# Optimization experiments

Measured on AMD Instinct MI355X. Metric: run time of the kernel, lower is better.

## Reference

```python
import jax, jax.numpy as jnp
import numpy as np

BATCH = 4096
DIM = 256
TEMP = 0.5
COS_EPS = 1e-8  # torch.nn.CosineSimilarity default eps


def setup_inputs() -> dict:
    key = jax.random.key(0)
    k1, k2 = jax.random.split(key)
    zis = jax.random.normal(k1, (BATCH, DIM), dtype=jnp.float32)
    zjs = jax.random.normal(k2, (BATCH, DIM), dtype=jnp.float32)
    return {"zis": zis, "zjs": zjs}


def reference(zis, zjs):
    n = zis.shape[0]  # batch_size
    # representations = cat([zjs, zis]) -> (2N, D)
    reps = jnp.concatenate([zjs, zis], axis=0)
    # cosine similarity matrix: dot / max(|x||y|, eps)  (matches torch CosineSimilarity)
    norms = jnp.linalg.norm(reps, axis=-1)  # (2N,)
    sim = (reps @ reps.T) / jnp.maximum(norms[:, None] * norms[None, :], COS_EPS)  # (2N, 2N)
    # positives: diag at offset +N (rows 0..N-1) then offset -N (rows N..2N-1)
    pos = jnp.concatenate([jnp.diagonal(sim, n), jnp.diagonal(sim, -n)])  # (2N,)
    # CE with label 0 over [pos, negatives]: negatives = row minus {diag, positive};
    # logsumexp([pos] + negatives) == logsumexp(row with only the self-diagonal masked),
    # since the positive appears exactly once in the row.
    two_n = 2 * n
    logits = sim / TEMP
    logits = jnp.where(jnp.eye(two_n, dtype=bool), -jnp.inf, logits)
    lse = jax.nn.logsumexp(logits, axis=-1)  # (2N,)
    loss = jnp.sum(lse - pos / TEMP)  # CrossEntropyLoss(reduction='sum')
    return loss / two_n
```

## Files before the change

kernel.cpp:

```cpp
#include <hip/hip_runtime.h>
#include <hip/hip_bf16.h>

#define TWO_N  8192
#define N_HALF 4096
#define DIMS   256

typedef __bf16 bf16x8 __attribute__((ext_vector_type(8)));
typedef float  f32x4  __attribute__((ext_vector_type(4)));
typedef unsigned short ushort8v __attribute__((ext_vector_type(8)));

__device__ __forceinline__ float fast_exp2(float x) {
#if __has_builtin(__builtin_amdgcn_exp2f)
    return __builtin_amdgcn_exp2f(x);
#else
    float r; asm("v_exp_f32 %0, %1" : "=v"(r) : "v"(x)); return r;
#endif
}

#define GLOAD_LDS16(g, l)                                                      \
    __builtin_amdgcn_global_load_lds(                                          \
        (const __attribute__((address_space(1))) unsigned int*)(g),            \
        (__attribute__((address_space(3))) unsigned int*)(l), 16, 0, 0)

__global__ __launch_bounds__(256) void nrm_kernel(const float* __restrict__ zis,
                                                  const float* __restrict__ zjs,
                                                  unsigned short* __restrict__ swz)
{
    const int tid = threadIdx.x;
    const int l32 = tid & 31;
    const int row = blockIdx.x * 8 + (tid >> 5);
    const int k0  = l32 * 8;

    const float* src = (row < N_HALF) ? (zjs + (size_t)row * DIMS)
                                      : (zis + (size_t)(row - N_HALF) * DIMS);
    const float4 v0 = reinterpret_cast<const float4*>(src + k0)[0];
    const float4 v1 = reinterpret_cast<const float4*>(src + k0 + 4)[0];
    float ss = v0.x * v0.x + v0.y * v0.y + v0.z * v0.z + v0.w * v0.w
             + v1.x * v1.x + v1.y * v1.y + v1.z * v1.z + v1.w * v1.w;
#pragma unroll
    for (int m = 1; m < 32; m <<= 1) ss += __shfl_xor(ss, m, 64);
    const float inv = rsqrtf(ss) * 1.69864360045f;

    const float vals[8] = {v0.x, v0.y, v0.z, v0.w, v1.x, v1.y, v1.z, v1.w};
    ushort8v o;
#pragma unroll
    for (int j = 0; j < 8; ++j) {
        __hip_bfloat16 b = __float2bfloat16(vals[j] * inv);
        o[j] = *reinterpret_cast<unsigned short*>(&b);
    }
    const int chunk = ((row >> 4) * 8 + (l32 >> 2)) * 64 + (l32 & 3) * 16 + (row & 15);
    *reinterpret_cast<ushort8v*>(swz + (size_t)chunk * 8) = o;
}

__global__ __launch_bounds__(512, 2) void ntx_kernel(const __bf16* __restrict__ swz,
                                                     float* __restrict__ rowsum_part,
                                                     float* __restrict__ pos_part)
{
    __shared__ __bf16 abuf[2][32768];

    const int lane = threadIdx.x & 63;
    const int wave = threadIdx.x >> 6;
    const int l15  = lane & 15;
    const int quad = lane >> 4;

    const int rg     = blockIdx.x & 15;
    const int cs     = blockIdx.x >> 4;
    const int wr0    = rg * 512 + wave * 64;
    const int p0     = wr0 ^ N_HALF;

    auto stage = [&](int buf, int c) {
        const __bf16* gsrc = swz + (size_t)(cs * 32 + c * 8 + wave) * 4096 + lane * 8;
#pragma unroll
        for (int h = 0; h < 8; ++h)
            GLOAD_LDS16(gsrc + h * 512, &abuf[buf][wave * 4096 + h * 512]);
    };

    stage(0, 0);

    bf16x8 bfrag[4][8];
#pragma unroll
    for (int t = 0; t < 4; ++t) {
        const __bf16* bp = swz + (size_t)((wr0 >> 4) + t) * 4096 + lane * 8;
#pragma unroll
        for (int kk = 0; kk < 8; ++kk)
            bfrag[t][kk] = *reinterpret_cast<const bf16x8*>(bp + kk * 512);
    }

    float sum_exp[4] = {0.f, 0.f, 0.f, 0.f};
    float pos_acc = 0.f;

    asm volatile("s_waitcnt vmcnt(0)" ::: "memory");
    __syncthreads();

    int cur = 0;
    for (int c = 0; c < 4; ++c) {
        if (c < 3) stage(cur ^ 1, c + 1);

        const int cc_base = cs * 512 + c * 128;

        auto compute = [&](const bf16x8* af, int it) {
            const int c0 = cc_base + it * 16;
            f32x4 acc[4] = {{0.f, 0.f, 0.f, 0.f}, {0.f, 0.f, 0.f, 0.f},
                            {0.f, 0.f, 0.f, 0.f}, {0.f, 0.f, 0.f, 0.f}};
#pragma unroll
            for (int kk = 0; kk < 8; ++kk) {
#pragma unroll
                for (int t = 0; t < 4; ++t)
                    acc[t] = __builtin_amdgcn_mfma_f32_16x16x32_bf16(
                        af[kk], bfrag[t][kk], acc[t], 0, 0, 0);
            }
            const bool special = (c0 < wr0 + 64 && c0 + 16 > wr0) ||
                                 (c0 < p0 + 64 && c0 + 16 > p0);
            if (!special) {
#pragma unroll
                for (int t = 0; t < 4; ++t)
#pragma unroll
                    for (int j = 0; j < 4; ++j)
                        sum_exp[t] += fast_exp2(acc[t][j]);
            } else {
#pragma unroll
                for (int t = 0; t < 4; ++t) {
                    const int r = wr0 + t * 16 + l15;
#pragma unroll
                    for (int j = 0; j < 4; ++j) {
                        const int col = c0 + quad * 4 + j;
                        const float e = fast_exp2(acc[t][j]);
                        sum_exp[t] += (col == r) ? 0.f : e;
                        if (col == (r ^ N_HALF)) pos_acc += acc[t][j];
                    }
                }
            }
        };

        bf16x8 a0[8], a1[8];
#pragma unroll
        for (int kk = 0; kk < 8; ++kk)
            a0[kk] = *reinterpret_cast<const bf16x8*>(&abuf[cur][kk * 512 + lane * 8]);

        for (int it = 0; it < 8; it += 2) {
#pragma unroll
            for (int kk = 0; kk < 8; ++kk)
                a1[kk] = *reinterpret_cast<const bf16x8*>(
                    &abuf[cur][(it + 1) * 4096 + kk * 512 + lane * 8]);
            compute(a0, it);
            if (it + 2 < 8) {
#pragma unroll
                for (int kk = 0; kk < 8; ++kk)
                    a0[kk] = *reinterpret_cast<const bf16x8*>(
                        &abuf[cur][(it + 2) * 4096 + kk * 512 + lane * 8]);
            }
            compute(a1, it + 1);
        }

        asm volatile("s_waitcnt vmcnt(0)" ::: "memory");
        __syncthreads();
        cur ^= 1;
    }

#pragma unroll
    for (int t = 0; t < 4; ++t) {
        float s = sum_exp[t];
        s += __shfl_xor(s, 16, 64);
        s += __shfl_xor(s, 32, 64);
        if (lane < 16)
            rowsum_part[(size_t)cs * TWO_N + wr0 + t * 16 + lane] = s;
    }

#pragma unroll
    for (int m = 1; m < 64; m <<= 1) pos_acc += __shfl_xor(pos_acc, m, 64);
    if (lane == 0) pos_part[blockIdx.x * 8 + wave] = pos_acc;
}

__global__ __launch_bounds__(1024) void fin1_kernel(const float* __restrict__ rowsum_part,
                                                    const float* __restrict__ pos_part,
                                                    float* __restrict__ block_part)
{
    __shared__ float red[16];
    const int t = threadIdx.x;
    const int r = blockIdx.x * 1024 + t;
    float acc = 0.f;
#pragma unroll
    for (int cs = 0; cs < 16; ++cs)
        acc += rowsum_part[(size_t)cs * TWO_N + r];
    float v = logf(acc);
    if (r < 2048)
        v -= 0.69314718055994531f * pos_part[r];
#pragma unroll
    for (int m = 1; m < 64; m <<= 1) v += __shfl_xor(v, m, 64);
    if ((t & 63) == 0) red[t >> 6] = v;
    __syncthreads();
    if (t == 0) {
        float s = 0.f;
#pragma unroll
        for (int w = 0; w < 16; ++w) s += red[w];
        block_part[blockIdx.x] = s;
    }
}

__global__ void fin2_kernel(const float* __restrict__ block_part, float* __restrict__ out)
{
    if (threadIdx.x == 0) {
        float s = 0.f;
#pragma unroll
        for (int i = 0; i < 8; ++i) s += block_part[i];
        out[0] = s / (float)TWO_N;
    }
}

extern "C" void kernel_launch(void* const* d_in, const int* in_sizes, int n_in,
                              void* d_out, int out_size, void* d_ws, size_t ws_size,
                              hipStream_t stream)
{
    const float* zis = (const float*)d_in[0];
    const float* zjs = (const float*)d_in[1];

    unsigned short* swz = (unsigned short*)d_ws;
    float* rowsum_part  = (float*)((char*)d_ws + (size_t)TWO_N * DIMS * sizeof(unsigned short));
    float* pos_part     = rowsum_part + (size_t)16 * TWO_N;
    float* block_part   = pos_part + 2048;

    nrm_kernel<<<TWO_N / 8, 256, 0, stream>>>(zis, zjs, swz);
    ntx_kernel<<<256, 512, 0, stream>>>((const __bf16*)swz, rowsum_part, pos_part);
    fin1_kernel<<<8, 1024, 0, stream>>>(rowsum_part, pos_part, block_part);
    fin2_kernel<<<1, 64, 0, stream>>>(block_part, (float*)d_out);
}
```

Measured before the change: 92.09 us.

## Switch similarity GEMM to 32x32x16 MFMA with matching swizzled bf16 layout

Replaces the 16x16x32 bf16 MFMA tiles with 32x32x16 MFMA tiles. Each wave now computes two 32x32 output blocks per column group, and the staged A columns are reused across both. The normalization kernel writes a new 32-row-group swizzled layout that matches the bigger MFMA operand fragments, and the diagonal/positive masking and row-sum reductions are remapped to the 32x32 accumulator layout. The aim is fewer MFMA instructions and less LDS fragment traffic per output, at the cost of more accumulator registers (two f32x16 plus 32 per-lane partial sums), which may pressure occupancy.

```diff
diff --git a/kernel.cpp b/kernel.cpp
--- a/kernel.cpp
+++ b/kernel.cpp
@@ -6,7 +6,7 @@
 #define DIMS   256
 
 typedef __bf16 bf16x8 __attribute__((ext_vector_type(8)));
-typedef float  f32x4  __attribute__((ext_vector_type(4)));
+typedef float  f32x16 __attribute__((ext_vector_type(16)));
 typedef unsigned short ushort8v __attribute__((ext_vector_type(8)));
 
 __device__ __forceinline__ float fast_exp2(float x) {
@@ -48,8 +48,9 @@
         __hip_bfloat16 b = __float2bfloat16(vals[j] * inv);
         o[j] = *reinterpret_cast<unsigned short*>(&b);
     }
-    const int chunk = ((row >> 4) * 8 + (l32 >> 2)) * 64 + (l32 & 3) * 16 + (row & 15);
-    *reinterpret_cast<ushort8v*>(swz + (size_t)chunk * 8) = o;
+    const size_t addr = ((size_t)((row >> 5) * 16 + (l32 >> 1)) * 64
+                         + (l32 & 1) * 32 + (row & 31)) * 8;
+    *reinterpret_cast<ushort8v*>(swz + addr) = o;
 }
 
 __global__ __launch_bounds__(512, 2) void ntx_kernel(const __bf16* __restrict__ swz,
@@ -60,33 +61,35 @@
 
     const int lane = threadIdx.x & 63;
     const int wave = threadIdx.x >> 6;
-    const int l15  = lane & 15;
-    const int quad = lane >> 4;
-
-    const int rg     = blockIdx.x & 15;
-    const int cs     = blockIdx.x >> 4;
-    const int wr0    = rg * 512 + wave * 64;
-    const int p0     = wr0 ^ N_HALF;
+    const int half = lane >> 5;
+    const int cl31 = lane & 31;
+
+    const int rg   = blockIdx.x & 15;
+    const int cs   = blockIdx.x >> 4;
+    const int wr0  = rg * 512 + wave * 64;
+    const int p0   = wr0 ^ N_HALF;
+    const int g0   = wr0 >> 5;
 
     auto stage = [&](int buf, int c) {
-        const __bf16* gsrc = swz + (size_t)(cs * 32 + c * 8 + wave) * 4096 + lane * 8;
+        const __bf16* gsrc = swz + ((size_t)(cs * 256 + c * 64 + wave * 8)) * 512 + lane * 8;
 #pragma unroll
         for (int h = 0; h < 8; ++h)
-            GLOAD_LDS16(gsrc + h * 512, &abuf[buf][wave * 4096 + h * 512]);
+            GLOAD_LDS16(gsrc + h * 512, &abuf[buf][(wave * 8 + h) * 512]);
     };
 
     stage(0, 0);
 
-    bf16x8 bfrag[4][8];
-#pragma unroll
-    for (int t = 0; t < 4; ++t) {
-        const __bf16* bp = swz + (size_t)((wr0 >> 4) + t) * 4096 + lane * 8;
-#pragma unroll
-        for (int kk = 0; kk < 8; ++kk)
-            bfrag[t][kk] = *reinterpret_cast<const bf16x8*>(bp + kk * 512);
-    }
-
-    float sum_exp[4] = {0.f, 0.f, 0.f, 0.f};
+    bf16x8 bfrag[2][16];
+#pragma unroll
+    for (int t = 0; t < 2; ++t)
+#pragma unroll
+        for (int ks = 0; ks < 16; ++ks)
+            bfrag[t][ks] = *reinterpret_cast<const bf16x8*>(
+                swz + (size_t)((g0 + t) * 16 + ks) * 512 + lane * 8);
+
+    float sums0[16], sums1[16];
+#pragma unroll
+    for (int g = 0; g < 16; ++g) { sums0[g] = 0.f; sums1[g] = 0.f; }
     float pos_acc = 0.f;
 
     asm volatile("s_waitcnt vmcnt(0)" ::: "memory");
@@ -96,60 +99,58 @@
     for (int c = 0; c < 4; ++c) {
         if (c < 3) stage(cur ^ 1, c + 1);
 
-        const int cc_base = cs * 512 + c * 128;
-
-        auto compute = [&](const bf16x8* af, int it) {
-            const int c0 = cc_base + it * 16;
-            f32x4 acc[4] = {{0.f, 0.f, 0.f, 0.f}, {0.f, 0.f, 0.f, 0.f},
-                            {0.f, 0.f, 0.f, 0.f}, {0.f, 0.f, 0.f, 0.f}};
-#pragma unroll
-            for (int kk = 0; kk < 8; ++kk) {
-#pragma unroll
-                for (int t = 0; t < 4; ++t)
-                    acc[t] = __builtin_amdgcn_mfma_f32_16x16x32_bf16(
-                        af[kk], bfrag[t][kk], acc[t], 0, 0, 0);
+        for (int cg = 0; cg < 4; ++cg) {
+            const int c0 = cs * 512 + c * 128 + cg * 32;
+            const __bf16* ab = &abuf[cur][cg * 16 * 512 + lane * 8];
+
+            f32x16 acc0, acc1;
+#pragma unroll
+            for (int g = 0; g < 16; ++g) { acc0[g] = 0.f; acc1[g] = 0.f; }
+
+            bf16x8 a[8];
+#pragma unroll
+            for (int ks = 0; ks < 8; ++ks)
+                a[ks] = *reinterpret_cast<const bf16x8*>(ab + ks * 512);
+#pragma unroll
+            for (int ks = 0; ks < 8; ++ks) {
+                acc0 = __builtin_amdgcn_mfma_f32_32x32x16_bf16(a[ks], bfrag[0][ks], acc0, 0, 0, 0);
+                acc1 = __builtin_amdgcn_mfma_f32_32x32x16_bf16(a[ks], bfrag[1][ks], acc1, 0, 0, 0);
             }
-            const bool special = (c0 < wr0 + 64 && c0 + 16 > wr0) ||
-                                 (c0 < p0 + 64 && c0 + 16 > p0);
+#pragma unroll
+            for (int ks = 0; ks < 8; ++ks)
+                a[ks] = *reinterpret_cast<const bf16x8*>(ab + (8 + ks) * 512);
+#pragma unroll
+            for (int ks = 0; ks < 8; ++ks) {
+                acc0 = __builtin_amdgcn_mfma_f32_32x32x16_bf16(a[ks], bfrag[0][8 + ks], acc0, 0, 0, 0);
+                acc1 = __builtin_amdgcn_mfma_f32_32x32x16_bf16(a[ks], bfrag[1][8 + ks], acc1, 0, 0, 0);
+            }
+
+            const bool special = (c0 < wr0 + 64 && c0 + 32 > wr0) ||
+                                 (c0 < p0 + 64 && c0 + 32 > p0);
             if (!special) {
 #pragma unroll
-                for (int t = 0; t < 4; ++t)
-#pragma unroll
-                    for (int j = 0; j < 4; ++j)
-                        sum_exp[t] += fast_exp2(acc[t][j]);
+                for (int g = 0; g < 16; ++g) {
+                    sums0[g] += fast_exp2(acc0[g]);
+                    sums1[g] += fast_exp2(acc1[g]);
+                }
             } else {
-#pragma unroll
-                for (int t = 0; t < 4; ++t) {
-                    const int r = wr0 + t * 16 + l15;
-#pragma unroll
-                    for (int j = 0; j < 4; ++j) {
-                        const int col = c0 + quad * 4 + j;
-                        const float e = fast_exp2(acc[t][j]);
-                        sum_exp[t] += (col == r) ? 0.f : e;
-                        if (col == (r ^ N_HALF)) pos_acc += acc[t][j];
+                const int r0 = wr0 + cl31;
+                const int r1 = wr0 + 32 + cl31;
+#pragma unroll
+                for (int g = 0; g < 16; ++g) {
+                    const int col = c0 + (g & 3) + 8 * (g >> 2) + 4 * half;
+                    {
+                        const float e = fast_exp2(acc0[g]);
+                        sums0[g] += (col == r0) ? 0.f : e;
+                        if (col == (r0 ^ N_HALF)) pos_acc += acc0[g];
+                    }
+                    {
+                        const float e = fast_exp2(acc1[g]);
+                        sums1[g] += (col == r1) ? 0.f : e;
+                        if (col == (r1 ^ N_HALF)) pos_acc += acc1[g];
                     }
                 }
             }
-        };
-
-        bf16x8 a0[8], a1[8];
-#pragma unroll
-        for (int kk = 0; kk < 8; ++kk)
-            a0[kk] = *reinterpret_cast<const bf16x8*>(&abuf[cur][kk * 512 + lane * 8]);
-
-        for (int it = 0; it < 8; it += 2) {
-#pragma unroll
-            for (int kk = 0; kk < 8; ++kk)
-                a1[kk] = *reinterpret_cast<const bf16x8*>(
-                    &abuf[cur][(it + 1) * 4096 + kk * 512 + lane * 8]);
-            compute(a0, it);
-            if (it + 2 < 8) {
-#pragma unroll
-                for (int kk = 0; kk < 8; ++kk)
-                    a0[kk] = *reinterpret_cast<const bf16x8*>(
-                        &abuf[cur][(it + 2) * 4096 + kk * 512 + lane * 8]);
-            }
-            compute(a1, it + 1);
         }
 
         asm volatile("s_waitcnt vmcnt(0)" ::: "memory");
@@ -157,13 +158,16 @@
         cur ^= 1;
     }
 
-#pragma unroll
-    for (int t = 0; t < 4; ++t) {
-        float s = sum_exp[t];
-        s += __shfl_xor(s, 16, 64);
-        s += __shfl_xor(s, 32, 64);
-        if (lane < 16)
-            rowsum_part[(size_t)cs * TWO_N + wr0 + t * 16 + lane] = s;
+    {
+        float s0 = 0.f, s1 = 0.f;
+#pragma unroll
+        for (int g = 0; g < 16; ++g) { s0 += sums0[g]; s1 += sums1[g]; }
+        s0 += __shfl_xor(s0, 32, 64);
+        s1 += __shfl_xor(s1, 32, 64);
+        if (lane < 32) {
+            rowsum_part[(size_t)cs * TWO_N + wr0 + cl31]      = s0;
+            rowsum_part[(size_t)cs * TWO_N + wr0 + 32 + cl31] = s1;
+        }
     }
 
 #pragma unroll
```

New measurement: 358.4 us. +289.2%, slower.
